# Kernel tuning notes

Measured on AMD Instinct MI355X. Metric: run time of the kernel, lower is better.

The kernel has to match this reference:

```python
import jax, jax.numpy as jnp
import numpy as np

BEV_X = 128
BEV_Y = 128
NUM_VOXELS = BEV_X * BEV_Y


def setup_inputs() -> dict:
    key = jax.random.key(0)
    k1, k2, k3 = jax.random.split(key, 3)
    B, N, D, H, W, C = 2, 6, 112, 16, 44, 80
    depth_logits = jax.random.normal(k1, (B, N, D, H, W), dtype=jnp.float32)
    context = jax.random.normal(k2, (B, N, C, H, W), dtype=jnp.float32)
    geom_idx = jax.random.randint(k3, (B, N, D, H, W), 0, NUM_VOXELS, dtype=jnp.int32)
    return {"depth_logits": depth_logits, "context": context, "geom_idx": geom_idx}


def reference(depth_logits, context, geom_idx):
    # depth_logits: [B,N,D,H,W], context: [B,N,C,H,W], geom_idx: [B,N,D,H,W] in [0, NUM_VOXELS)
    B, N, D, H, W = depth_logits.shape
    C = context.shape[2]
    # softmax over depth bins -> per-pixel depth distribution
    depth = jax.nn.softmax(depth_logits, axis=2)
    # lift: outer product depth x context -> [B,N,D,H,W,C]
    feat = jnp.einsum('bndhw,bnchw->bndhwc', depth, context)
    P = N * D * H * W
    feat = feat.reshape(B * P, C)
    # splat: scatter-add each frustum point into its BEV voxel (batch-offset indices)
    idx = (geom_idx.reshape(B, P) + jnp.arange(B, dtype=jnp.int32)[:, None] * NUM_VOXELS).reshape(-1)
    bev = jax.ops.segment_sum(feat, idx, num_segments=B * NUM_VOXELS)
    # [B, C, BEV_Y, BEV_X]
    return bev.reshape(B, BEV_Y, BEV_X, C).transpose(0, 3, 1, 2)
```

## Files before the change

kernel.cpp:

```cpp
#include <hip/hip_runtime.h>
#include <hip/hip_bf16.h>


constexpr int B = 2, N = 6, D = 112, H = 16, W = 44, C = 80;
constexpr int HW = H * W;
constexpr int NPIX = B * N * HW;
constexpr int NV = 128 * 128;
constexpr int PTS = NPIX * D;
constexpr int DHW = D * HW;
constexpr int NBKT = 512;
constexpr int CAP = 2816;
constexpr int RPB = 16 * D;

__global__ __launch_bounds__(256) void ctxT_kernel(
    const float* __restrict__ ctx, float* __restrict__ ctxT,
    int* __restrict__ cursor) {
  const int t = threadIdx.x;
  if (blockIdx.x < 2) cursor[blockIdx.x * 256 + t] = 0;

  __shared__ float tile[C][65];
  const int pix0 = blockIdx.x * 64;
  const int bn = pix0 / HW;
  const int hw0 = pix0 - bn * HW;

  const float* src = ctx + (size_t)bn * C * HW + hw0;
#pragma unroll
  for (int it = 0; it < (C * 64) / 256; ++it) {
    const int idx = it * 256 + t;
    const int c = idx >> 6;
    const int i = idx & 63;
    tile[c][i] = src[(size_t)c * HW + i];
  }
  __syncthreads();
  float* dst = ctxT + (size_t)pix0 * C;
#pragma unroll
  for (int it = 0; it < (C * 64) / 256; ++it) {
    const int j = it * 256 + t;
    const int pl = j / C;
    const int c = j - pl * C;
    dst[j] = tile[c][pl];
  }
}

__global__ __launch_bounds__(256) void scatter_kernel(
    const float* __restrict__ logits, const int* __restrict__ gidx,
    int* __restrict__ cursor, uint2* __restrict__ sorted) {
  const int t = threadIdx.x;
  const int blk = blockIdx.x;
  const int bn = blk / 44;
  const int hw0 = (blk - bn * 44) * 16;
  const int b = bn / N;
  const int pix0 = bn * HW + hw0;

  __shared__ float redm[16][17], reds[16][17];
  __shared__ int hist[256], sbase[256], soff[256];
  __shared__ int wsum[4];
  __shared__ uint2 srec[RPB];

  hist[t] = 0;

  const int l = t & 15;
  const int q = t >> 4;
  const size_t base = (size_t)bn * DHW + hw0 + l;

  float x[7];
  float m = -3.0e38f;
#pragma unroll
  for (int j = 0; j < 7; ++j) {
    x[j] = logits[base + (size_t)(q * 7 + j) * HW];
    m = fmaxf(m, x[j]);
  }
  redm[l][q] = m;
  __syncthreads();
#pragma unroll
  for (int qq = 0; qq < 16; ++qq) m = fmaxf(m, redm[l][qq]);
  float s = 0.0f;
#pragma unroll
  for (int j = 0; j < 7; ++j) {
    x[j] = __expf(x[j] - m);
    s += x[j];
  }
  reds[l][q] = s;
  __syncthreads();
  s = 0.0f;
#pragma unroll
  for (int qq = 0; qq < 16; ++qq) s += reds[l][qq];
  const float inv = 1.0f / s;

  unsigned w0[7];
  int rank[7];
#pragma unroll
  for (int j = 0; j < 7; ++j) {
    const int fb = b * NV + gidx[base + (size_t)(q * 7 + j) * HW];
    w0[j] = (unsigned)(pix0 + l) | ((unsigned)fb << 16);
    x[j] *= inv;
    rank[j] = atomicAdd(&hist[(w0[j] >> 22) & 255], 1);
  }
  __syncthreads();

  const int hv = hist[t];
  int xx = hv;
#pragma unroll
  for (int o = 1; o < 64; o <<= 1) {
    const int y = __shfl_up(xx, o, 64);
    if ((t & 63) >= o) xx += y;
  }
  if ((t & 63) == 63) wsum[t >> 6] = xx;
  sbase[t] = hv ? atomicAdd(&cursor[(b << 8) | t], hv) : 0;
  __syncthreads();
  int woff = 0;
#pragma unroll
  for (int ww = 0; ww < 4; ++ww)
    if (ww < (t >> 6)) woff += wsum[ww];
  soff[t] = woff + xx - hv;
  __syncthreads();

#pragma unroll
  for (int j = 0; j < 7; ++j) {
    const int lb = (w0[j] >> 22) & 255;
    srec[soff[lb] + rank[j]] = make_uint2(w0[j], __float_as_uint(x[j]));
  }
  __syncthreads();

  for (int s_ = t; s_ < RPB; s_ += 256) {
    const uint2 r = srec[s_];
    const int gb = (r.x >> 22) & 511;
    const int lb = gb & 255;
    const int posin = sbase[lb] + (s_ - soff[lb]);
    if (posin < CAP)
      sorted[(size_t)gb * CAP + posin] = r;
  }
}

__global__ __launch_bounds__(1024) void gather_kernel(
    const float* __restrict__ ctxT, const uint2* __restrict__ sorted,
    const int* __restrict__ cursor, float* __restrict__ out) {
  const int t = threadIdx.x;
  const int g = blockIdx.x;
  const int b = g >> 8;
  const int vox0 = (g & 255) * 64;

  __shared__ uint2 srec[CAP];
  __shared__ float tile[64][80];
  __shared__ int shist[64], soff[64];

  if (t < 64) shist[t] = 0;
  __syncthreads();

  int cnt = cursor[g];
  if (cnt > CAP) cnt = CAP;
  const uint2* rec = sorted + (size_t)g * CAP;

  uint2 rr[3];
  int rk[3];
#pragma unroll
  for (int k = 0; k < 3; ++k) {
    const int idx = t + k * 1024;
    rk[k] = -1;
    if (idx < cnt) {
      rr[k] = rec[idx];
      rk[k] = atomicAdd(&shist[(rr[k].x >> 16) & 63], 1);
    }
  }
  __syncthreads();

  if (t < 64) {
    const int v = shist[t];
    int xx = v;
#pragma unroll
    for (int o = 1; o < 64; o <<= 1) {
      const int y = __shfl_up(xx, o, 64);
      if (t >= o) xx += y;
    }
    soff[t] = xx - v;
  }
  __syncthreads();

#pragma unroll
  for (int k = 0; k < 3; ++k) {
    if (rk[k] >= 0) {
      const int v = (rr[k].x >> 16) & 63;
      srec[soff[v] + rk[k]] = rr[k];
    }
  }
  __syncthreads();

  const int w = t >> 6;
  const int l = t & 63;
  for (int j = 0; j < 4; ++j) {
    const int v = w * 4 + j;
    const int s0 = soff[v];
    const int n = shist[v];
    float a0 = 0.0f, a1 = 0.0f;
    int k = 0;
    for (; k + 4 <= n; k += 4) {
      const uint2 ra = srec[s0 + k + 0];
      const uint2 rb = srec[s0 + k + 1];
      const uint2 rc = srec[s0 + k + 2];
      const uint2 rd = srec[s0 + k + 3];
      const float* wa = ctxT + (size_t)(ra.x & 0xFFFFu) * C;
      const float* wb = ctxT + (size_t)(rb.x & 0xFFFFu) * C;
      const float* wc = ctxT + (size_t)(rc.x & 0xFFFFu) * C;
      const float* wd = ctxT + (size_t)(rd.x & 0xFFFFu) * C;
      const float pa = __uint_as_float(ra.y);
      const float pb = __uint_as_float(rb.y);
      const float pc = __uint_as_float(rc.y);
      const float pd = __uint_as_float(rd.y);
      a0 += pa * wa[l];
      a0 += pb * wb[l];
      a0 += pc * wc[l];
      a0 += pd * wd[l];
      if (l < 16) {
        a1 += pa * wa[64 + l];
        a1 += pb * wb[64 + l];
        a1 += pc * wc[64 + l];
        a1 += pd * wd[64 + l];
      }
    }
    for (; k < n; ++k) {
      const uint2 ra = srec[s0 + k];
      const float* wa = ctxT + (size_t)(ra.x & 0xFFFFu) * C;
      const float pa = __uint_as_float(ra.y);
      a0 += pa * wa[l];
      if (l < 16) a1 += pa * wa[64 + l];
    }
    tile[v][l] = a0;
    if (l < 16) tile[v][64 + l] = a1;
  }
  __syncthreads();

  const size_t ob = (size_t)b * C * NV + vox0;
#pragma unroll
  for (int i = 0; i < 5; ++i) {
    const int idx = i * 1024 + t;
    const int c = idx >> 6;
    const int v = idx & 63;
    out[ob + (size_t)c * NV + v] = tile[v][c];
  }
}

__global__ __launch_bounds__(256) void lift_splat_direct_kernel(
    const float* __restrict__ logits, const float* __restrict__ ctx,
    const int* __restrict__ gidx, float* __restrict__ out) {
  const int t = threadIdx.x;
  const int pix = blockIdx.x;
  const int hw = pix % HW;
  const int bn = pix / HW;
  const int b = bn / N;

  const float* lg = logits + (size_t)bn * DHW + hw;
  const int* gi = gidx + (size_t)bn * DHW + hw;
  const float* cx = ctx + (size_t)bn * (C * HW) + hw;

  __shared__ float s_prob[D];
  __shared__ float s_ctx[C];
  __shared__ int s_idx[D];
  __shared__ float red[256];

  float v = -3.0e38f;
  if (t < D) {
    v = lg[(size_t)t * HW];
    s_idx[t] = gi[(size_t)t * HW];
  }
  if (t < C) s_ctx[t] = cx[(size_t)t * HW];

  red[t] = v;
  __syncthreads();
#pragma unroll
  for (int s = 128; s >= 1; s >>= 1) {
    if (t < s) red[t] = fmaxf(red[t], red[t + s]);
    __syncthreads();
  }
  const float m = red[0];
  __syncthreads();

  const float e = (t < D) ? __expf(v - m) : 0.0f;
  red[t] = e;
  __syncthreads();
#pragma unroll
  for (int s = 128; s >= 1; s >>= 1) {
    if (t < s) red[t] += red[t + s];
    __syncthreads();
  }
  const float inv = 1.0f / red[0];
  if (t < D) s_prob[t] = e * inv;
  __syncthreads();

  for (int f = t; f < D * C; f += 256) {
    const int d = f / C;
    const int c = f - d * C;
    atomicAdd(&out[((size_t)(b * C + c)) * NV + s_idx[d]],
              s_prob[d] * s_ctx[c]);
  }
}

extern "C" void kernel_launch(void* const* d_in, const int* in_sizes, int n_in,
                              void* d_out, int out_size, void* d_ws,
                              size_t ws_size, hipStream_t stream) {
  const float* logits = (const float*)d_in[0];
  const float* ctx = (const float*)d_in[1];
  const int* gidx = (const int*)d_in[2];
  float* out = (float*)d_out;

  size_t off = 0;
  uint2* sorted = (uint2*)((char*)d_ws + off);
  off += (size_t)NBKT * CAP * sizeof(uint2);
  float* ctxT = (float*)((char*)d_ws + off);
  off += (size_t)NPIX * C * sizeof(float);
  int* cursor = (int*)((char*)d_ws + off);
  off += (size_t)NBKT * sizeof(int);

  if (ws_size >= off) {
    ctxT_kernel<<<NPIX / 64, 256, 0, stream>>>(ctx, ctxT, cursor);
    scatter_kernel<<<B * N * (HW / 16), 256, 0, stream>>>(logits, gidx,
                                                          cursor, sorted);
    gather_kernel<<<NBKT, 1024, 0, stream>>>(ctxT, sorted, cursor, out);
  } else {
    (void)hipMemsetAsync(d_out, 0, (size_t)out_size * sizeof(float), stream);
    lift_splat_direct_kernel<<<NPIX, 256, 0, stream>>>(logits, ctx, gidx, out);
  }
}
```

Measured before the change: 103.0 us.

## Pack splat records into 32 bits with 12-bit probabilities and fuse the context transpose

Each sorted record shrinks from a uint2 to one 32-bit word. The word holds a 6-bit in-bucket voxel, a 14-bit pixel index and a 12-bit quantized softmax probability; the bucket id now comes from the block's position. This halves the bytes the scatter and gather kernels move through global memory and LDS. The context transpose is folded into the scatter kernel, and the cursor reset becomes a memset, removing one kernel launch. The risk is accuracy: probabilities near 1/112 quantized with a step of 1/4095 carry a relative error of a few percent, which may break the reference tolerance.

```diff
diff --git a/kernel.cpp b/kernel.cpp
--- a/kernel.cpp
+++ b/kernel.cpp
@@ -6,45 +6,15 @@
 constexpr int HW = H * W;
 constexpr int NPIX = B * N * HW;
 constexpr int NV = 128 * 128;
-constexpr int PTS = NPIX * D;
 constexpr int DHW = D * HW;
 constexpr int NBKT = 512;
 constexpr int CAP = 2816;
 constexpr int RPB = 16 * D;
 
-__global__ __launch_bounds__(256) void ctxT_kernel(
-    const float* __restrict__ ctx, float* __restrict__ ctxT,
-    int* __restrict__ cursor) {
-  const int t = threadIdx.x;
-  if (blockIdx.x < 2) cursor[blockIdx.x * 256 + t] = 0;
-
-  __shared__ float tile[C][65];
-  const int pix0 = blockIdx.x * 64;
-  const int bn = pix0 / HW;
-  const int hw0 = pix0 - bn * HW;
-
-  const float* src = ctx + (size_t)bn * C * HW + hw0;
-#pragma unroll
-  for (int it = 0; it < (C * 64) / 256; ++it) {
-    const int idx = it * 256 + t;
-    const int c = idx >> 6;
-    const int i = idx & 63;
-    tile[c][i] = src[(size_t)c * HW + i];
-  }
-  __syncthreads();
-  float* dst = ctxT + (size_t)pix0 * C;
-#pragma unroll
-  for (int it = 0; it < (C * 64) / 256; ++it) {
-    const int j = it * 256 + t;
-    const int pl = j / C;
-    const int c = j - pl * C;
-    dst[j] = tile[c][pl];
-  }
-}
-
 __global__ __launch_bounds__(256) void scatter_kernel(
-    const float* __restrict__ logits, const int* __restrict__ gidx,
-    int* __restrict__ cursor, uint2* __restrict__ sorted) {
+    const float* __restrict__ logits, const float* __restrict__ ctx,
+    const int* __restrict__ gidx, float* __restrict__ ctxT,
+    int* __restrict__ cursor, unsigned* __restrict__ sorted) {
   const int t = threadIdx.x;
   const int blk = blockIdx.x;
   const int bn = blk / 44;
@@ -52,12 +22,34 @@
   const int b = bn / N;
   const int pix0 = bn * HW + hw0;
 
+  __shared__ float tile[16][81];
   __shared__ float redm[16][17], reds[16][17];
   __shared__ int hist[256], sbase[256], soff[256];
   __shared__ int wsum[4];
-  __shared__ uint2 srec[RPB];
+  __shared__ unsigned srec[RPB];
+  __shared__ unsigned char sbkt[RPB];
 
   hist[t] = 0;
+
+  const float* csrc = ctx + (size_t)bn * C * HW + hw0;
+#pragma unroll
+  for (int it = 0; it < (16 * C) / 256; ++it) {
+    const int idx = it * 256 + t;
+    const int c = idx >> 4;
+    const int i = idx & 15;
+    tile[i][c] = csrc[(size_t)c * HW + i];
+  }
+  __syncthreads();
+  {
+    float* dst = ctxT + (size_t)pix0 * C;
+#pragma unroll
+    for (int it = 0; it < (16 * C) / 256; ++it) {
+      const int j = it * 256 + t;
+      const int p = j / C;
+      const int c = j - p * C;
+      dst[j] = tile[p][c];
+    }
+  }
 
   const int l = t & 15;
   const int q = t >> 4;
@@ -87,14 +79,15 @@
   for (int qq = 0; qq < 16; ++qq) s += reds[l][qq];
   const float inv = 1.0f / s;
 
-  unsigned w0[7];
-  int rank[7];
+  unsigned key[7];
+  int lb7[7], rank[7];
 #pragma unroll
   for (int j = 0; j < 7; ++j) {
     const int fb = b * NV + gidx[base + (size_t)(q * 7 + j) * HW];
-    w0[j] = (unsigned)(pix0 + l) | ((unsigned)fb << 16);
-    x[j] *= inv;
-    rank[j] = atomicAdd(&hist[(w0[j] >> 22) & 255], 1);
+    const unsigned p12 = __float2uint_rn(x[j] * inv * 4095.0f);
+    key[j] = ((unsigned)(fb & 63) << 26) | ((unsigned)(pix0 + l) << 12) | p12;
+    lb7[j] = (fb >> 6) & 255;
+    rank[j] = atomicAdd(&hist[lb7[j]], 1);
   }
   __syncthreads();
 
@@ -117,30 +110,29 @@
 
 #pragma unroll
   for (int j = 0; j < 7; ++j) {
-    const int lb = (w0[j] >> 22) & 255;
-    srec[soff[lb] + rank[j]] = make_uint2(w0[j], __float_as_uint(x[j]));
+    const int slot = soff[lb7[j]] + rank[j];
+    srec[slot] = key[j];
+    sbkt[slot] = (unsigned char)lb7[j];
   }
   __syncthreads();
 
   for (int s_ = t; s_ < RPB; s_ += 256) {
-    const uint2 r = srec[s_];
-    const int gb = (r.x >> 22) & 511;
-    const int lb = gb & 255;
+    const int lb = sbkt[s_];
     const int posin = sbase[lb] + (s_ - soff[lb]);
     if (posin < CAP)
-      sorted[(size_t)gb * CAP + posin] = r;
+      sorted[(size_t)((b << 8) | lb) * CAP + posin] = srec[s_];
   }
 }
 
 __global__ __launch_bounds__(1024) void gather_kernel(
-    const float* __restrict__ ctxT, const uint2* __restrict__ sorted,
+    const float* __restrict__ ctxT, const unsigned* __restrict__ sorted,
     const int* __restrict__ cursor, float* __restrict__ out) {
   const int t = threadIdx.x;
   const int g = blockIdx.x;
   const int b = g >> 8;
   const int vox0 = (g & 255) * 64;
 
-  __shared__ uint2 srec[CAP];
+  __shared__ unsigned srec[CAP];
   __shared__ float tile[64][80];
   __shared__ int shist[64], soff[64];
 
@@ -149,9 +141,9 @@
 
   int cnt = cursor[g];
   if (cnt > CAP) cnt = CAP;
-  const uint2* rec = sorted + (size_t)g * CAP;
-
-  uint2 rr[3];
+  const unsigned* rec = sorted + (size_t)g * CAP;
+
+  unsigned rr[3];
   int rk[3];
 #pragma unroll
   for (int k = 0; k < 3; ++k) {
@@ -159,7 +151,7 @@
     rk[k] = -1;
     if (idx < cnt) {
       rr[k] = rec[idx];
-      rk[k] = atomicAdd(&shist[(rr[k].x >> 16) & 63], 1);
+      rk[k] = atomicAdd(&shist[rr[k] >> 26], 1);
     }
   }
   __syncthreads();
@@ -178,13 +170,11 @@
 
 #pragma unroll
   for (int k = 0; k < 3; ++k) {
-    if (rk[k] >= 0) {
-      const int v = (rr[k].x >> 16) & 63;
-      srec[soff[v] + rk[k]] = rr[k];
-    }
-  }
-  __syncthreads();
-
+    if (rk[k] >= 0) srec[soff[rr[k] >> 26] + rk[k]] = rr[k];
+  }
+  __syncthreads();
+
+  constexpr float QS = 1.0f / 4095.0f;
   const int w = t >> 6;
   const int l = t & 63;
   for (int j = 0; j < 4; ++j) {
@@ -194,18 +184,18 @@
     float a0 = 0.0f, a1 = 0.0f;
     int k = 0;
     for (; k + 4 <= n; k += 4) {
-      const uint2 ra = srec[s0 + k + 0];
-      const uint2 rb = srec[s0 + k + 1];
-      const uint2 rc = srec[s0 + k + 2];
-      const uint2 rd = srec[s0 + k + 3];
-      const float* wa = ctxT + (size_t)(ra.x & 0xFFFFu) * C;
-      const float* wb = ctxT + (size_t)(rb.x & 0xFFFFu) * C;
-      const float* wc = ctxT + (size_t)(rc.x & 0xFFFFu) * C;
-      const float* wd = ctxT + (size_t)(rd.x & 0xFFFFu) * C;
-      const float pa = __uint_as_float(ra.y);
-      const float pb = __uint_as_float(rb.y);
-      const float pc = __uint_as_float(rc.y);
-      const float pd = __uint_as_float(rd.y);
+      const unsigned ra = srec[s0 + k + 0];
+      const unsigned rb = srec[s0 + k + 1];
+      const unsigned rc = srec[s0 + k + 2];
+      const unsigned rd = srec[s0 + k + 3];
+      const float* wa = ctxT + (size_t)((ra >> 12) & 0x3FFFu) * C;
+      const float* wb = ctxT + (size_t)((rb >> 12) & 0x3FFFu) * C;
+      const float* wc = ctxT + (size_t)((rc >> 12) & 0x3FFFu) * C;
+      const float* wd = ctxT + (size_t)((rd >> 12) & 0x3FFFu) * C;
+      const float pa = (float)(ra & 0xFFFu) * QS;
+      const float pb = (float)(rb & 0xFFFu) * QS;
+      const float pc = (float)(rc & 0xFFFu) * QS;
+      const float pd = (float)(rd & 0xFFFu) * QS;
       a0 += pa * wa[l];
       a0 += pb * wb[l];
       a0 += pc * wc[l];
@@ -218,9 +208,9 @@
       }
     }
     for (; k < n; ++k) {
-      const uint2 ra = srec[s0 + k];
-      const float* wa = ctxT + (size_t)(ra.x & 0xFFFFu) * C;
-      const float pa = __uint_as_float(ra.y);
+      const unsigned ra = srec[s0 + k];
+      const float* wa = ctxT + (size_t)((ra >> 12) & 0x3FFFu) * C;
+      const float pa = (float)(ra & 0xFFFu) * QS;
       a0 += pa * wa[l];
       if (l < 16) a1 += pa * wa[64 + l];
     }
@@ -303,17 +293,17 @@
   float* out = (float*)d_out;
 
   size_t off = 0;
-  uint2* sorted = (uint2*)((char*)d_ws + off);
-  off += (size_t)NBKT * CAP * sizeof(uint2);
+  unsigned* sorted = (unsigned*)((char*)d_ws + off);
+  off += (size_t)NBKT * CAP * sizeof(unsigned);
   float* ctxT = (float*)((char*)d_ws + off);
   off += (size_t)NPIX * C * sizeof(float);
   int* cursor = (int*)((char*)d_ws + off);
   off += (size_t)NBKT * sizeof(int);
 
   if (ws_size >= off) {
-    ctxT_kernel<<<NPIX / 64, 256, 0, stream>>>(ctx, ctxT, cursor);
-    scatter_kernel<<<B * N * (HW / 16), 256, 0, stream>>>(logits, gidx,
-                                                          cursor, sorted);
+    (void)hipMemsetAsync(cursor, 0, (size_t)NBKT * sizeof(int), stream);
+    scatter_kernel<<<B * N * (HW / 16), 256, 0, stream>>>(
+        logits, ctx, gidx, ctxT, cursor, sorted);
     gather_kernel<<<NBKT, 1024, 0, stream>>>(ctxT, sorted, cursor, out);
   } else {
     (void)hipMemsetAsync(d_out, 0, (size_t)out_size * sizeof(float), stream);
```

Result: no change. 103.4 us (+0.4%).
